# Kernel tuning notes

Hardware: AMD Instinct MI355X
Metric: run time of the kernel (lower is better)

## Reference

```python
import jax, jax.numpy as jnp
import numpy as np

N, W, D, IC, OC, R = 256, 1, 64, 32, 32, 8


def setup_inputs() -> dict:
    key = jax.random.key(0)
    k1, k2 = jax.random.split(key)
    x = jax.random.normal(k1, (N, W, D, IC, R), dtype=jnp.float32)
    weights = jax.random.normal(k2, (D, IC, OC, R), dtype=jnp.float32)
    return {"x": x, "weights": weights}


def reference(x, weights):
    # x: [n, w, d, ic, r] -> [n, w, d, ic, 1, r]
    # weights: [d, ic, oc, r] -> broadcast as [1, 1, d, ic, oc, r]
    # out: logsumexp over ic -> [n, w, d, oc, r]
    logits = x[:, :, :, :, None, :] + weights[None, None]
    return jax.nn.logsumexp(logits, axis=3)
```

## Files before the change

kernel.cpp:

```cpp
#include <hip/hip_runtime.h>


constexpr int kN = 256, kD = 64, kIC = 32, kOC = 32, kR = 8;
constexpr int kNT = 16;
constexpr int PAD = 36;

__global__ __launch_bounds__(256) void lse_kernel(
    const float* __restrict__ x, const float* __restrict__ w,
    float* __restrict__ out)
{
    __shared__ __align__(16) float ws[kIC * kR * PAD];
    __shared__ __align__(16) float xs[kNT * kR * PAD];

    const int t  = threadIdx.x;
    const int d  = blockIdx.x;
    const int n0 = blockIdx.y * kNT;

    {
        const float4* wg = reinterpret_cast<const float4*>(w + (size_t)d * (kIC * kOC * kR));
        #pragma unroll
        for (int i = 0; i < 8; ++i) {
            float4 v = wg[i * 256 + t];
            int lin = (i * 256 + t) * 4;
            int ic = lin >> 8;
            int oc = (lin >> 3) & 31;
            int r  = lin & 7;
            float* p = &ws[(ic * kR + r) * PAD + oc];
            p[0 * PAD] = __expf(v.x);
            p[1 * PAD] = __expf(v.y);
            p[2 * PAD] = __expf(v.z);
            p[3 * PAD] = __expf(v.w);
        }
    }

    {
        #pragma unroll
        for (int i = 0; i < 4; ++i) {
            int fidx = i * 256 + t;
            int ns = fidx >> 6;
            int e  = fidx & 63;
            const float4* xg = reinterpret_cast<const float4*>(
                x + (size_t)(n0 + ns) * (kD * kIC * kR) + (size_t)d * (kIC * kR));
            float4 v = xg[e];
            int lin = e * 4;
            int ic = lin >> 3;
            int r  = lin & 7;
            float* p = &xs[(ns * kR + r) * PAD + ic];
            p[0 * PAD] = __expf(v.x);
            p[1 * PAD] = __expf(v.y);
            p[2 * PAD] = __expf(v.z);
            p[3 * PAD] = __expf(v.w);
        }
    }

    __syncthreads();

    const int rr  = t & 7;
    const int ocq = (t >> 3) & 7;
    const int nq  = t >> 6;

    float acc[4][4];
    #pragma unroll
    for (int jj = 0; jj < 4; ++jj)
        #pragma unroll
        for (int k = 0; k < 4; ++k)
            acc[jj][k] = 0.f;

    const float4* xs4 = reinterpret_cast<const float4*>(xs);
    #pragma unroll
    for (int icq = 0; icq < 8; ++icq) {
        float4 xv[4];
        #pragma unroll
        for (int jj = 0; jj < 4; ++jj)
            xv[jj] = xs4[((nq * 4 + jj) * kR + rr) * (PAD / 4) + icq];
        #pragma unroll
        for (int q = 0; q < 4; ++q) {
            const int ic = icq * 4 + q;
            float wv[4];
            #pragma unroll
            for (int k = 0; k < 4; ++k)
                wv[k] = ws[(ic * kR + rr) * PAD + k * 8 + ocq];
            #pragma unroll
            for (int jj = 0; jj < 4; ++jj) {
                const float* xvp = reinterpret_cast<const float*>(&xv[jj]);
                const float xq = xvp[q];
                #pragma unroll
                for (int k = 0; k < 4; ++k)
                    acc[jj][k] = fmaf(xq, wv[k], acc[jj][k]);
            }
        }
    }

    #pragma unroll
    for (int jj = 0; jj < 4; ++jj) {
        const int n = n0 + nq * 4 + jj;
        float* op = out + (size_t)n * (kD * kOC * kR) + (size_t)d * (kOC * kR) + rr;
        #pragma unroll
        for (int k = 0; k < 4; ++k)
            op[(k * 8 + ocq) * 8] = __logf(acc[jj][k]);
    }
}

extern "C" void kernel_launch(void* const* d_in, const int* in_sizes, int n_in,
                              void* d_out, int out_size, void* d_ws, size_t ws_size,
                              hipStream_t stream) {
    const float* x = (const float*)d_in[0];
    const float* w = (const float*)d_in[1];
    float* out = (float*)d_out;
    dim3 grid(kD, kN / kNT);
    lse_kernel<<<grid, 256, 0, stream>>>(x, w, out);
}
```

Measured before the change: 15.26 us.

## Double batch tile and widen per-thread OC tile with permuted weight layout

```diff
diff --git a/kernel.cpp b/kernel.cpp
--- a/kernel.cpp
+++ b/kernel.cpp
@@ -2,8 +2,9 @@
 
 
 constexpr int kN = 256, kD = 64, kIC = 32, kOC = 32, kR = 8;
-constexpr int kNT = 16;
+constexpr int kNT = 32;
 constexpr int PAD = 36;
+constexpr int PQ  = PAD / 4;
 
 __global__ __launch_bounds__(256) void lse_kernel(
     const float* __restrict__ x, const float* __restrict__ w,
@@ -20,12 +21,14 @@
         const float4* wg = reinterpret_cast<const float4*>(w + (size_t)d * (kIC * kOC * kR));
         #pragma unroll
         for (int i = 0; i < 8; ++i) {
-            float4 v = wg[i * 256 + t];
-            int lin = (i * 256 + t) * 4;
-            int ic = lin >> 8;
-            int oc = (lin >> 3) & 31;
-            int r  = lin & 7;
-            float* p = &ws[(ic * kR + r) * PAD + oc];
+            const int qg = i * 256 + t;
+            float4 v = wg[qg];
+            const int lin = qg * 4;
+            const int ic = lin >> 8;
+            const int oc = (lin >> 3) & 31;
+            const int r0 = lin & 7;
+            const int j  = (oc & 3) * 8 + (oc >> 2);
+            float* p = &ws[(ic * kR + r0) * PAD + j];
             p[0 * PAD] = __expf(v.x);
             p[1 * PAD] = __expf(v.y);
             p[2 * PAD] = __expf(v.z);
@@ -35,17 +38,16 @@
 
     {
         #pragma unroll
-        for (int i = 0; i < 4; ++i) {
-            int fidx = i * 256 + t;
-            int ns = fidx >> 6;
-            int e  = fidx & 63;
+        for (int i = 0; i < 8; ++i) {
+            const int fidx = i * 256 + t;
+            const int nl = fidx >> 6;
+            const int e  = fidx & 63;
             const float4* xg = reinterpret_cast<const float4*>(
-                x + (size_t)(n0 + ns) * (kD * kIC * kR) + (size_t)d * (kIC * kR));
+                x + (size_t)(n0 + nl) * (kD * kIC * kR) + (size_t)d * (kIC * kR));
             float4 v = xg[e];
-            int lin = e * 4;
-            int ic = lin >> 3;
-            int r  = lin & 7;
-            float* p = &xs[(ns * kR + r) * PAD + ic];
+            const int ic = e >> 1;
+            const int r0 = (e & 1) * 4;
+            float* p = &xs[(nl * kR + r0) * PAD + ic];
             p[0 * PAD] = __expf(v.x);
             p[1 * PAD] = __expf(v.y);
             p[2 * PAD] = __expf(v.z);
@@ -56,48 +58,54 @@
     __syncthreads();
 
     const int rr  = t & 7;
-    const int ocq = (t >> 3) & 7;
-    const int nq  = t >> 6;
+    const int och = (t >> 3) & 3;
+    const int ng  = t >> 5;
 
-    float acc[4][4];
+    float acc[4][8];
     #pragma unroll
     for (int jj = 0; jj < 4; ++jj)
         #pragma unroll
-        for (int k = 0; k < 4; ++k)
+        for (int k = 0; k < 8; ++k)
             acc[jj][k] = 0.f;
 
     const float4* xs4 = reinterpret_cast<const float4*>(xs);
+    const float4* ws4 = reinterpret_cast<const float4*>(ws);
+
     #pragma unroll
     for (int icq = 0; icq < 8; ++icq) {
         float4 xv[4];
         #pragma unroll
         for (int jj = 0; jj < 4; ++jj)
-            xv[jj] = xs4[((nq * 4 + jj) * kR + rr) * (PAD / 4) + icq];
+            xv[jj] = xs4[((ng * 4 + jj) * kR + rr) * PQ + icq];
         #pragma unroll
         for (int q = 0; q < 4; ++q) {
             const int ic = icq * 4 + q;
-            float wv[4];
-            #pragma unroll
-            for (int k = 0; k < 4; ++k)
-                wv[k] = ws[(ic * kR + rr) * PAD + k * 8 + ocq];
+            const float4 w0 = ws4[(ic * kR + rr) * PQ + och * 2];
+            const float4 w1 = ws4[(ic * kR + rr) * PQ + och * 2 + 1];
             #pragma unroll
             for (int jj = 0; jj < 4; ++jj) {
-                const float* xvp = reinterpret_cast<const float*>(&xv[jj]);
-                const float xq = xvp[q];
-                #pragma unroll
-                for (int k = 0; k < 4; ++k)
-                    acc[jj][k] = fmaf(xq, wv[k], acc[jj][k]);
+                const float* xp = reinterpret_cast<const float*>(&xv[jj]);
+                const float xq = xp[q];
+                acc[jj][0] = fmaf(xq, w0.x, acc[jj][0]);
+                acc[jj][1] = fmaf(xq, w0.y, acc[jj][1]);
+                acc[jj][2] = fmaf(xq, w0.z, acc[jj][2]);
+                acc[jj][3] = fmaf(xq, w0.w, acc[jj][3]);
+                acc[jj][4] = fmaf(xq, w1.x, acc[jj][4]);
+                acc[jj][5] = fmaf(xq, w1.y, acc[jj][5]);
+                acc[jj][6] = fmaf(xq, w1.z, acc[jj][6]);
+                acc[jj][7] = fmaf(xq, w1.w, acc[jj][7]);
             }
         }
     }
 
     #pragma unroll
     for (int jj = 0; jj < 4; ++jj) {
-        const int n = n0 + nq * 4 + jj;
-        float* op = out + (size_t)n * (kD * kOC * kR) + (size_t)d * (kOC * kR) + rr;
+        const int n = n0 + ng * 4 + jj;
+        float* op = out + (size_t)n * (kD * kOC * kR) + (size_t)d * (kOC * kR)
+                    + och * 8 + rr;
         #pragma unroll
-        for (int k = 0; k < 4; ++k)
-            op[(k * 8 + ocq) * 8] = __logf(acc[jj][k]);
+        for (int k = 0; k < 8; ++k)
+            op[k * 32] = __logf(acc[jj][k]);
     }
 }
 
```

Measured after the change: 15.03 us. Within noise of the previous version (-1.5%).
